# Kernel optimization log

Measured on AMD Instinct MI355X. Metric: run time of the kernel, lower is better.

## Reference

```python
import jax, jax.numpy as jnp
import numpy as np

LEAK = 0.95
NUM_STEPS = 10
THR = 1.0  # all layers get threshold = 1.0 in __init__

@jax.custom_vjp
def spike(x):
    # Surrogate_BP_Function.forward: heaviside(x > 0)
    return (x > 0).astype(x.dtype)

def _spike_fwd(x):
    return spike(x), x

def _spike_bwd(x, g):
    # backward: grad * 0.3 * relu(1 - |x|)
    return (g * 0.3 * jnp.maximum(1.0 - jnp.abs(x), 0.0),)

spike.defvjp(_spike_fwd, _spike_bwd)

def conv3x3(x, w):
    # stride 1, padding 1, no bias, NCHW / OIHW
    return jax.lax.conv_general_dilated(
        x, w, window_strides=(1, 1), padding=[(1, 1), (1, 1)],
        dimension_numbers=('NCHW', 'OIHW', 'NCHW'))

def avgpool2(x):
    b, c, h, w = x.shape
    return x.reshape(b, c, h // 2, 2, w // 2, 2).mean(axis=(3, 5))

def setup_inputs() -> dict:
    key = jax.random.key(0)
    ks = jax.random.split(key, 11)
    def w(k, shape, scale):
        return jax.random.normal(k, shape, dtype=jnp.float32) * scale
    inp = jax.random.normal(ks[0], (128, 3, 32, 32), dtype=jnp.float32)
    return {
        'inp': inp,
        'w1': w(ks[1], (64, 3, 3, 3), 0.35),
        'w2': w(ks[2], (64, 64, 3, 3), 0.1),
        'w3': w(ks[3], (128, 64, 3, 3), 0.1),
        'w4': w(ks[4], (128, 128, 3, 3), 0.08),
        'w5': w(ks[5], (256, 128, 3, 3), 0.08),
        'w6': w(ks[6], (256, 256, 3, 3), 0.06),
        'w7': w(ks[7], (256, 256, 3, 3), 0.06),
        'fc1_w': w(ks[8], (1024, 4096), 0.03),   # Linear(4*4*256, 1024)
        'fc2_w': w(ks[9], (10, 1024), 0.05),     # Linear(1024, 10)
    }

def reference(inp, w1, w2, w3, w4, w5, w6, w7, fc1_w, fc2_w):
    batch = inp.shape[0]
    conv_ws = [w2, w3, w4, w5, w6, w7]          # layers i = 1..6
    pool_after = [True, False, True, False, False, True]  # pool1 after i=1, pool2 after i=3, pool3 after i=6
    static = conv3x3(inp, w1)                   # static_input = conv1(inp)

    def step(carry, _):
        mem0, mem_fc1, mem_fc2 = carry
        # LIF update for conv1 (leaky accumulation of static input)
        mem0 = (1.0 - LEAK) * mem0 + LEAK * static
        thr = mem0 / THR - 1.0
        out_prev = spike(thr)
        mem0 = mem0 - jnp.where(thr > 0, THR, 0.0)  # soft reset
        # conv layers 2..7: membrane is OVERWRITTEN by the conv output each step
        for j, w in enumerate(conv_ws):
            m = conv3x3(out_prev, w)
            thr = m / THR - 1.0
            out_prev = spike(thr)
            if pool_after[j]:
                out_prev = avgpool2(out_prev)
        flat = out_prev.reshape(batch, -1)      # [B, 256*4*4]
        mem_fc1 = (1.0 - LEAK) * mem_fc1 + LEAK * (flat @ fc1_w.T)
        thr = mem_fc1 / THR - 1.0
        out = spike(thr)
        mem_fc1 = mem_fc1 - jnp.where(thr > 0, THR, 0.0)
        mem_fc2 = mem_fc2 + out @ fc2_w.T
        return (mem0, mem_fc1, mem_fc2), None

    init = (jnp.zeros_like(static),
            jnp.zeros((batch, 1024), dtype=inp.dtype),
            jnp.zeros((batch, fc2_w.shape[0]), dtype=inp.dtype))
    (mem0, mem_fc1, mem_fc2), _ = jax.lax.scan(step, init, None, length=NUM_STEPS)
    return mem_fc2 / NUM_STEPS
```

## Files before the change

kernel.cpp:

```cpp
#include <hip/hip_runtime.h>


typedef __attribute__((ext_vector_type(4))) int int32x4;

__device__ __forceinline__ float bf2f(ushort h) {
    union { unsigned u; float f; } v; v.u = ((unsigned)h) << 16;
    return v.f;
}
constexpr int ilog2(int x) { int r = 0; while (x > 1) { x >>= 1; ++r; } return r; }

__device__ __forceinline__ void gl_lds16(const void* g, void* l) {
    __builtin_amdgcn_global_load_lds(
        (const __attribute__((address_space(1))) unsigned int*)g,
        (__attribute__((address_space(3))) unsigned int*)l, 16, 0, 0);
}

#define SC21 4.76837158203125e-07
#define SC23 1.1920928955078125e-07

template <int IC, int OC>
__global__ void prep_convw_i8_k(const float* __restrict__ w, char* __restrict__ dst) {
    int idx = blockIdx.x * 256 + threadIdx.x;
    if (idx >= OC * IC * 9) return;
    int oc = idx / (IC * 9);
    int rem = idx % (IC * 9);
    int ic = rem / 9, q = rem % 9;
    int wq_ = (int)rintf(w[idx] * 2097152.0f);
    int a2 = ((wq_ + 128) & 255) - 128;
    int t2 = (wq_ - a2) >> 8;
    int a1 = ((t2 + 128) & 255) - 128;
    int a0 = (t2 - a1) >> 8;
    int sg = ic >> 6, kin = ic & 63, c = kin >> 4, bb = kin & 15;
    int oct = oc >> 6, ocl = oc & 63;
    constexpr int OCT = OC / 64;
    size_t base = ((size_t)(sg * 9 + q) * OCT + oct) * 12288;
    char digs[3] = {(char)a0, (char)a1, (char)a2};
#pragma unroll
    for (int s = 0; s < 3; ++s)
        dst[base + (size_t)(c * 192 + s * 64 + ocl) * 16 + bb] = digs[s];
}

__global__ void prep_fc1w_i8_k(const float* __restrict__ w, char* __restrict__ dst) {
    int idx = blockIdx.x * 256 + threadIdx.x;
    if (idx >= 1024 * 4096) return;
    int j = idx >> 12, k = idx & 4095;
    int c = k >> 4, hw = k & 15;
    int kp = hw * 256 + c;
    int wq_ = (int)rintf(w[idx] * 2097152.0f);
    int a2 = ((wq_ + 128) & 255) - 128;
    int t2 = (wq_ - a2) >> 8;
    int a1 = ((t2 + 128) & 255) - 128;
    int a0 = (t2 - a1) >> 8;
    int slab = kp >> 6, kin = kp & 63, cch = kin >> 4, bb = kin & 15;
    int oct = j >> 6, ocl = j & 63;
    size_t base = ((size_t)(slab * 16 + oct)) * 12288;
    char digs[3] = {(char)a0, (char)a1, (char)a2};
#pragma unroll
    for (int s = 0; s < 3; ++s)
        dst[base + (size_t)(cch * 192 + s * 64 + ocl) * 16 + bb] = digs[s];
}

template <int H, int C>
__global__ void halo0_k(char* __restrict__ buf) {
    constexpr int P = 4 * H + 4;
    constexpr int CPI = P * (C / 16);
    int idx = blockIdx.x * 256 + threadIdx.x;
    if (idx >= 1280 * CPI) return;
    int n = idx / CPI, r = idx % CPI;
    int p = r / (C / 16), c16 = r % (C / 16);
    int row, col;
    if (p < 2 * (H + 2)) { row = (p < H + 2) ? 0 : H + 1; col = p % (H + 2); }
    else { int qq = p - 2 * (H + 2); col = (qq < H) ? 0 : H + 1; row = 1 + (qq % H); }
    *(uint4*)&buf[(((size_t)n * (H + 2) + row) * (H + 2) + col) * C + c16 * 16] =
        (uint4){0u, 0u, 0u, 0u};
}

__global__ __launch_bounds__(256) void conv1lif_k(const float* __restrict__ inp,
                                                  const float* __restrict__ w1,
                                                  char* __restrict__ act1) {
    __shared__ float ws[27 * 64];
    for (int e = threadIdx.x; e < 1728; e += 256) {
        int oc = e / 27, j = e % 27;
        ws[j * 64 + oc] = w1[e];
    }
    __syncthreads();
    int t = blockIdx.x * 256 + threadIdx.x;
    int q = t & 3;
    int m = t >> 2;
    int n = m >> 10, h = (m >> 5) & 31, w = m & 31;
    float xv[27];
#pragma unroll
    for (int ic = 0; ic < 3; ++ic)
#pragma unroll
        for (int kh = 0; kh < 3; ++kh)
#pragma unroll
            for (int kw = 0; kw < 3; ++kw) {
                int r = h + kh - 1, c = w + kw - 1;
                xv[ic * 9 + kh * 3 + kw] =
                    (r >= 0 && r < 32 && c >= 0 && c < 32)
                        ? inp[(n * 3 + ic) * 1024 + r * 32 + c] : 0.0f;
            }
    float s[16], mem[16];
#pragma unroll
    for (int o = 0; o < 16; ++o) { s[o] = 0.f; mem[o] = 0.f; }
#pragma unroll
    for (int j = 0; j < 27; ++j) {
        float x = xv[j];
        const float* wr = &ws[j * 64 + q * 16];
#pragma unroll
        for (int o = 0; o < 16; ++o) s[o] += wr[o] * x;
    }
    const size_t dbase = (((size_t)h + 1) * 34 + (w + 1)) * 64 + q * 16;
    for (int st = 0; st < 10; ++st) {
        unsigned r[4];
#pragma unroll
        for (int g = 0; g < 4; ++g) {
            unsigned acc = 0;
#pragma unroll
            for (int e = 0; e < 4; ++e) {
                int o = g * 4 + e;
                mem[o] = 0.05f * mem[o] + 0.95f * s[o];
                unsigned b = (mem[o] > 1.f) ? 1u : 0u;
                mem[o] -= (float)b;
                acc |= b << (8 * e);
            }
            r[g] = acc;
        }
        size_t d = ((size_t)(st * 128 + n) * 34 * 34) * 64 + dbase;
        *(uint4*)&act1[d] = (uint4){r[0], r[1], r[2], r[3]};
    }
}

template <int H, int W, int IC, int OC, int NI, int MR, int EPI>
__global__ __launch_bounds__(256) void convi8_k(const char* __restrict__ act,
                                                const char* __restrict__ wq,
                                                char* __restrict__ outs,
                                                float scale) {
    constexpr int PW = W + 2, PHR = MR + 2;
    constexpr int MBLK = NI * MR * W;
    constexpr int NPIX = NI * PHR * PW;
    constexpr int ACH = NPIX * 4;
    constexpr int HR = (ACH + 255) / 256;
    constexpr int SLABS = IC / 64;
    constexpr int OCT = OC / 64;
    constexpr int LHW = ilog2(H * W), LW2 = ilog2(W), LMW = ilog2(MR * W);
    static_assert(MBLK == 128, "tile mapping");

    __shared__ __align__(16) char sA[NPIX * 64];
    __shared__ __align__(16) char sB[2][12288];

    const int tid = threadIdx.x, lane = tid & 63;
    const int wid = tid >> 6, wm = wid >> 1, wn = wid & 1;
    const int b = blockIdx.x, oct = blockIdx.y;
    const int oc0 = oct * 64;
    const int m0 = b * MBLK;
    constexpr int TPI = (NI == 1) ? (H / MR) : 1;
    const int n0 = (NI == 1) ? (b / TPI) : (b * NI);
    const int h0 = (NI == 1) ? (b % TPI) * MR : 0;

    int asrc[HR]; bool apred[HR];
#pragma unroll
    for (int r = 0; r < HR; ++r) {
        int i = r * 256 + tid;
        apred[r] = (i < ACH);
        int ii = apred[r] ? i : 0;
        int c = ii / NPIX, pix = ii % NPIX;
        int pc = pix % PW, t2 = pix / PW;
        int hp = t2 % PHR, img = t2 / PHR;
        asrc[r] = (((n0 + img) * (H + 2) + h0 + hp) * PW + pc) * IC + c * 16;
    }
    int apix[4];
#pragma unroll
    for (int am = 0; am < 4; ++am) {
        int p = wm * 64 + am * 16 + (lane & 15);
        int img = p >> LMW;
        int pi = p & ((MR * W) - 1);
        int h = pi >> LW2;
        apix[am] = (img * PHR + h) * PW + (pi & (W - 1));
    }
    const int cA = lane >> 4;

    int32x4 acc[3][4][2];
#pragma unroll
    for (int s = 0; s < 3; ++s)
#pragma unroll
        for (int a = 0; a < 4; ++a)
#pragma unroll
            for (int bn = 0; bn < 2; ++bn) acc[s][a][bn] = (int32x4){0, 0, 0, 0};

    const size_t wqoct = (size_t)oct * 12288;
    int buf = 0;
    {
#pragma unroll
        for (int r = 0; r < HR; ++r)
            if (apred[r]) gl_lds16(act + asrc[r], sA + (r * 256 + tid) * 16);
        const char* wsrc = wq + wqoct + tid * 16;
#pragma unroll
        for (int r = 0; r < 3; ++r)
            gl_lds16(wsrc + r * 4096, sB[0] + (r * 256 + tid) * 16);
    }
    __syncthreads();

    for (int sl = 0; sl < SLABS; ++sl) {
        for (int q = 0; q < 9; ++q) {
            if (q < 8) {
                const char* wsrc = wq + (size_t)(sl * 9 + q + 1) * OCT * 12288 + wqoct + tid * 16;
#pragma unroll
                for (int r = 0; r < 3; ++r)
                    gl_lds16(wsrc + r * 4096, sB[buf ^ 1] + (r * 256 + tid) * 16);
            }
            const int qr = q / 3, qc = q % 3;
            int32x4 af[4];
#pragma unroll
            for (int am = 0; am < 4; ++am) {
                int pix = apix[am] + qr * PW + qc;
                af[am] = *(const int32x4*)&sA[(cA * NPIX + pix) * 16];
            }
#pragma unroll
            for (int s = 0; s < 3; ++s)
#pragma unroll
                for (int bn = 0; bn < 2; ++bn) {
                    int R = s * 64 + wn * 32 + bn * 16 + (lane & 15);
                    int32x4 bf = *(const int32x4*)&sB[buf][(cA * 192 + R) * 16];
#pragma unroll
                    for (int am = 0; am < 4; ++am)
                        acc[s][am][bn] = __builtin_amdgcn_mfma_i32_16x16x64_i8(
                            af[am], bf, acc[s][am][bn], 0, 0, 0);
                }
            if (q < 8) {
                __syncthreads();
                buf ^= 1;
            }
        }
        if (sl + 1 < SLABS) {
            const int sg2 = sl + 1;
            __syncthreads();
#pragma unroll
            for (int r = 0; r < HR; ++r)
                if (apred[r]) gl_lds16(act + asrc[r] + sg2 * 64, sA + (r * 256 + tid) * 16);
            const char* wsrc = wq + (size_t)(sg2 * 9) * OCT * 12288 + wqoct + tid * 16;
#pragma unroll
            for (int r = 0; r < 3; ++r)
                gl_lds16(wsrc + r * 4096, sB[buf ^ 1] + (r * 256 + tid) * 16);
            __syncthreads();
            buf ^= 1;
        }
    }

    const double dscale = (double)scale;
#pragma unroll
    for (int am = 0; am < 4; ++am)
#pragma unroll
        for (int bn = 0; bn < 2; ++bn)
#pragma unroll
            for (int rr = 0; rr < 4; ++rr) {
                int rl = wm * 64 + am * 16 + (lane >> 4) * 4 + rr;
                int col = oc0 + wn * 32 + bn * 16 + (lane & 15);
                int m = m0 + rl;
                float v = (float)((65536.0 * (double)acc[0][am][bn][rr]
                                 + 256.0 * (double)acc[1][am][bn][rr]
                                 + (double)acc[2][am][bn][rr]) * dscale);
                char sp = (v > 1.0f) ? (char)1 : (char)0;
                if (EPI == 1) {
                    int n = m >> LHW, h = (m >> LW2) & (H - 1), w = m & (W - 1);
                    outs[((size_t)(n * (H + 2) + h + 1) * PW + (w + 1)) * OC + col] = sp;
                } else {
                    outs[(size_t)m * OC + col] = sp;
                }
            }
}

template <int C, int HI>
__global__ void pool_i8_k(const char* __restrict__ in, char* __restrict__ out) {
    constexpr int HO = HI / 2, C16 = C / 16;
    constexpr int TOT = 1280 * HO * HO * C16;
    int idx = blockIdx.x * 256 + threadIdx.x;
    if (idx >= TOT) return;
    int c16 = idx % C16;
    int t = idx / C16;
    int w = t % HO; t /= HO;
    int h = t % HO;
    int n = t / HO;
    const char* p = in + ((size_t)(n * HI + 2 * h) * HI + 2 * w) * C + c16 * 16;
    uint4 a0 = *(const uint4*)p;
    uint4 a1 = *(const uint4*)(p + C);
    uint4 a2 = *(const uint4*)(p + (size_t)HI * C);
    uint4 a3 = *(const uint4*)(p + (size_t)HI * C + C);
    uint4 r;
    r.x = a0.x + a1.x + a2.x + a3.x;
    r.y = a0.y + a1.y + a2.y + a3.y;
    r.z = a0.z + a1.z + a2.z + a3.z;
    r.w = a0.w + a1.w + a2.w + a3.w;
    *(uint4*)&out[((size_t)(n * (HO + 2) + h + 1) * (HO + 2) + (w + 1)) * C + c16 * 16] = r;
}

__global__ void pool3q_k(const char* __restrict__ in, char* __restrict__ out) {
    int idx = blockIdx.x * 256 + threadIdx.x;
    if (idx >= 327680) return;
    int c16 = idx & 15;
    int t = idx >> 4;
    int wo = t & 3, ho = (t >> 2) & 3, n = t >> 4;
    const char* p = in + ((size_t)(n * 8 + 2 * ho) * 8 + 2 * wo) * 256 + c16 * 16;
    uint4 a0 = *(const uint4*)p;
    uint4 a1 = *(const uint4*)(p + 256);
    uint4 a2 = *(const uint4*)(p + 2048);
    uint4 a3 = *(const uint4*)(p + 2048 + 256);
    uint4 r;
    r.x = a0.x + a1.x + a2.x + a3.x;
    r.y = a0.y + a1.y + a2.y + a3.y;
    r.z = a0.z + a1.z + a2.z + a3.z;
    r.w = a0.w + a1.w + a2.w + a3.w;
    *(uint4*)&out[((size_t)(n * 16 + ho * 4 + wo) * 16 + c16) * 16] = r;
}

__global__ __launch_bounds__(256) void fc1i8_k(const char* __restrict__ A,
                                               const char* __restrict__ wq,
                                               float* __restrict__ part) {
    __shared__ __align__(16) char sA[2][8192];
    __shared__ __align__(16) char sB[2][12288];
    const int tid = threadIdx.x, lane = tid & 63;
    const int wid = tid >> 6, wm = wid >> 1, wn = wid & 1;
    const int m0 = blockIdx.x * 128, oct = blockIdx.y, kt = blockIdx.z;

    int32x4 acc[3][4][2];
#pragma unroll
    for (int s = 0; s < 3; ++s)
#pragma unroll
        for (int a = 0; a < 4; ++a)
#pragma unroll
            for (int bn = 0; bn < 2; ++bn) acc[s][a][bn] = (int32x4){0, 0, 0, 0};

    auto stageA = [&](int sg, int bf_) {
#pragma unroll
        for (int r = 0; r < 2; ++r) {
            int i = r * 256 + tid;
            int c = i >> 7, pix = i & 127;
            gl_lds16(A + (size_t)(m0 + pix) * 4096 + sg * 64 + c * 16,
                     sA[bf_] + (size_t)i * 16);
        }
    };
    auto stageB = [&](int sg, int bf_) {
        const char* src = wq + ((size_t)(sg * 16 + oct)) * 12288 + tid * 16;
#pragma unroll
        for (int r = 0; r < 3; ++r)
            gl_lds16(src + r * 4096, sB[bf_] + (r * 256 + tid) * 16);
    };

    int buf = 0;
    stageA(kt * 32, 0);
    stageB(kt * 32, 0);
    __syncthreads();
    const int cA = lane >> 4;
    for (int sl = 0; sl < 32; ++sl) {
        int sg = kt * 32 + sl;
        if (sl < 31) { stageA(sg + 1, buf ^ 1); stageB(sg + 1, buf ^ 1); }
        int32x4 af[4];
#pragma unroll
        for (int am = 0; am < 4; ++am)
            af[am] = *(const int32x4*)&sA[buf][(cA * 128 + wm * 64 + am * 16 + (lane & 15)) * 16];
#pragma unroll
        for (int s = 0; s < 3; ++s)
#pragma unroll
            for (int bn = 0; bn < 2; ++bn) {
                int R = s * 64 + wn * 32 + bn * 16 + (lane & 15);
                int32x4 bf = *(const int32x4*)&sB[buf][(cA * 192 + R) * 16];
#pragma unroll
                for (int am = 0; am < 4; ++am)
                    acc[s][am][bn] = __builtin_amdgcn_mfma_i32_16x16x64_i8(
                        af[am], bf, acc[s][am][bn], 0, 0, 0);
            }
        if (sl < 31) { __syncthreads(); buf ^= 1; }
    }
#pragma unroll
    for (int am = 0; am < 4; ++am)
#pragma unroll
        for (int bn = 0; bn < 2; ++bn)
#pragma unroll
            for (int rr = 0; rr < 4; ++rr) {
                int row = m0 + wm * 64 + am * 16 + (lane >> 4) * 4 + rr;
                int col = oct * 64 + wn * 32 + bn * 16 + (lane & 15);
                float v = (float)((65536.0 * (double)acc[0][am][bn][rr]
                                 + 256.0 * (double)acc[1][am][bn][rr]
                                 + (double)acc[2][am][bn][rr]) * SC23);
                part[((size_t)kt * 1280 + row) * 1024 + col] = v;
            }
}

__global__ void fc1lif_k(const float* __restrict__ part, ushort* __restrict__ sbuf) {
    int idx = blockIdx.x * 256 + threadIdx.x;
    int n = idx >> 10, j = idx & 1023;
    float m = 0.f;
    for (int t = 0; t < 10; ++t) {
        size_t row = (size_t)(t * 128 + n) * 1024 + j;
        float y = part[row] + part[1310720 + row];
        m = 0.05f * m + 0.95f * y;
        float sp = (m > 1.f) ? 1.f : 0.f;
        m -= sp;
        sbuf[row] = sp > 0.f ? (ushort)0x3F80 : (ushort)0;
    }
}

__global__ __launch_bounds__(256) void fc2o_k(const ushort* __restrict__ S,
                                              const float* __restrict__ W2,
                                              float* __restrict__ out) {
    __shared__ float wsh[10 * 1024];
    __shared__ float red[10][256];
    int n = blockIdx.x, tid = threadIdx.x;
    for (int e = tid; e < 10240; e += 256) wsh[e] = W2[e];
    __syncthreads();
    float accv = 0.f;
    for (int t = 0; t < 10; ++t) {
        const ushort* sp = S + ((size_t)(t * 128 + n)) * 1024 + tid * 4;
        float s0 = bf2f(sp[0]), s1 = bf2f(sp[1]), s2 = bf2f(sp[2]), s3 = bf2f(sp[3]);
#pragma unroll
        for (int o = 0; o < 10; ++o) {
            const float* w = &wsh[o * 1024 + tid * 4];
            red[o][tid] = s0 * w[0] + s1 * w[1] + s2 * w[2] + s3 * w[3];
        }
        __syncthreads();
        for (int off = 128; off >= 1; off >>= 1) {
            if (tid < off) {
#pragma unroll
                for (int o = 0; o < 10; ++o) red[o][tid] += red[o][tid + off];
            }
            __syncthreads();
        }
        if (tid < 10) accv += red[tid][0];
        __syncthreads();
    }
    if (tid < 10) out[n * 10 + tid] = accv * 0.1f;
}

extern "C" void kernel_launch(void* const* d_in, const int* in_sizes, int n_in,
                              void* d_out, int out_size, void* d_ws, size_t ws_size,
                              hipStream_t stream) {
    const float* inp  = (const float*)d_in[0];
    const float* w1   = (const float*)d_in[1];
    const float* w2   = (const float*)d_in[2];
    const float* w3   = (const float*)d_in[3];
    const float* w4   = (const float*)d_in[4];
    const float* w5   = (const float*)d_in[5];
    const float* w6   = (const float*)d_in[6];
    const float* w7   = (const float*)d_in[7];
    const float* fc1w = (const float*)d_in[8];
    const float* fc2w = (const float*)d_in[9];
    float* out = (float*)d_out;

    char* base = (char*)d_ws;
    char* arenaA = base;
    char* arenaB = base + 94679040;
    size_t o = 94679040 + 83886080;
    auto alloc = [&](size_t bytes) { void* p = base + o; o += (bytes + 255) & ~(size_t)255; return p; };
    char*   wq2  = (char*)alloc(110592);
    char*   wq3  = (char*)alloc(221184);
    char*   wq4  = (char*)alloc(442368);
    char*   wq5  = (char*)alloc(884736);
    char*   wq6  = (char*)alloc(1769472);
    char*   wq7  = (char*)alloc(1769472);
    char*   wqf1 = (char*)alloc(12582912);
    ushort* sbuf = (ushort*)alloc(2621440);
    (void)ws_size;

    char*  act1  = arenaA;
    char*  c2out = arenaB;
    char*  act2  = arenaA;
    char*  c3out = arenaB;
    char*  c4out = arenaA;
    char*  act3  = arenaA + 41943040;
    char*  c5out = arenaB;
    char*  c6out = arenaB + 33554432;
    char*  c7out = arenaA;
    char*  afc1  = arenaA + 20971520;
    float* part  = (float*)(arenaA + 26214400);

    prep_convw_i8_k<64, 64>  <<<(36864 + 255) / 256, 256, 0, stream>>>(w2, wq2);
    prep_convw_i8_k<64, 128> <<<(73728 + 255) / 256, 256, 0, stream>>>(w3, wq3);
    prep_convw_i8_k<128, 128><<<(147456 + 255) / 256, 256, 0, stream>>>(w4, wq4);
    prep_convw_i8_k<128, 256><<<(294912 + 255) / 256, 256, 0, stream>>>(w5, wq5);
    prep_convw_i8_k<256, 256><<<(589824 + 255) / 256, 256, 0, stream>>>(w6, wq6);
    prep_convw_i8_k<256, 256><<<(589824 + 255) / 256, 256, 0, stream>>>(w7, wq7);
    prep_fc1w_i8_k<<<(4194304 + 255) / 256, 256, 0, stream>>>(fc1w, wqf1);

    halo0_k<32, 64><<<(1280 * 132 * 4 + 255) / 256, 256, 0, stream>>>(act1);
    conv1lif_k<<<2048, 256, 0, stream>>>(inp, w1, act1);

    convi8_k<32, 32, 64, 64, 1, 4, 0>
        <<<dim3(10240, 1), 256, 0, stream>>>(act1, wq2, c2out, (float)SC21);
    halo0_k<16, 64><<<(1280 * 68 * 4 + 255) / 256, 256, 0, stream>>>(act2);
    pool_i8_k<64, 32><<<(1280 * 256 * 4 + 255) / 256, 256, 0, stream>>>(c2out, act2);

    halo0_k<16, 128><<<(1280 * 68 * 8 + 255) / 256, 256, 0, stream>>>(c3out);
    convi8_k<16, 16, 64, 128, 1, 8, 1>
        <<<dim3(2560, 2), 256, 0, stream>>>(act2, wq3, c3out, (float)SC23);
    convi8_k<16, 16, 128, 128, 1, 8, 0>
        <<<dim3(2560, 2), 256, 0, stream>>>(c3out, wq4, c4out, (float)SC21);
    halo0_k<8, 128><<<(1280 * 36 * 8 + 255) / 256, 256, 0, stream>>>(act3);
    pool_i8_k<128, 16><<<(1280 * 64 * 8 + 255) / 256, 256, 0, stream>>>(c4out, act3);

    halo0_k<8, 256><<<(1280 * 36 * 16 + 255) / 256, 256, 0, stream>>>(c5out);
    convi8_k<8, 8, 128, 256, 2, 8, 1>
        <<<dim3(640, 4), 256, 0, stream>>>(act3, wq5, c5out, (float)SC23);
    halo0_k<8, 256><<<(1280 * 36 * 16 + 255) / 256, 256, 0, stream>>>(c6out);
    convi8_k<8, 8, 256, 256, 2, 8, 1>
        <<<dim3(640, 4), 256, 0, stream>>>(c5out, wq6, c6out, (float)SC21);
    convi8_k<8, 8, 256, 256, 2, 8, 0>
        <<<dim3(640, 4), 256, 0, stream>>>(c6out, wq7, c7out, (float)SC21);

    pool3q_k<<<(327680 + 255) / 256, 256, 0, stream>>>(c7out, afc1);

    fc1i8_k<<<dim3(10, 16, 2), 256, 0, stream>>>(afc1, wqf1, part);
    fc1lif_k<<<512, 256, 0, stream>>>(part, sbuf);
    fc2o_k<<<128, 256, 0, stream>>>(sbuf, fc2w, out);
}
```

Baseline: 899.3 us.

## Triple-buffer conv weight tiles with a flattened loop and manual waitcnt barriers

The int8 conv kernel's weight staging moves from double to triple buffering, with prefetch two steps ahead. The slab/tap double loop becomes a single flattened loop. __syncthreads is replaced by explicit vmcnt waits plus s_barrier, so each iteration needs only one barrier instead of two. MFMA issue is wrapped in s_setprio. The extra 12KB of LDS per block may reduce occupancy, and the hand-written waitcnt counts must match the number of outstanding loads exactly.

```diff
diff --git a/kernel.cpp b/kernel.cpp
--- a/kernel.cpp
+++ b/kernel.cpp
@@ -143,11 +143,12 @@
     constexpr int HR = (ACH + 255) / 256;
     constexpr int SLABS = IC / 64;
     constexpr int OCT = OC / 64;
+    constexpr int U = SLABS * 9;
     constexpr int LHW = ilog2(H * W), LW2 = ilog2(W), LMW = ilog2(MR * W);
     static_assert(MBLK == 128, "tile mapping");
 
     __shared__ __align__(16) char sA[NPIX * 64];
-    __shared__ __align__(16) char sB[2][12288];
+    __shared__ __align__(16) char sB[3][12288];
 
     const int tid = threadIdx.x, lane = tid & 63;
     const int wid = tid >> 6, wm = wid >> 1, wn = wid & 1;
@@ -189,65 +190,62 @@
             for (int bn = 0; bn < 2; ++bn) acc[s][a][bn] = (int32x4){0, 0, 0, 0};
 
     const size_t wqoct = (size_t)oct * 12288;
-    int buf = 0;
-    {
+
+    auto stage_B = [&](int u_) {
+        const char* wsrc = wq + (size_t)u_ * (OCT * 12288) + wqoct + tid * 16;
+        char* d = sB[u_ % 3] + tid * 16;
+        gl_lds16(wsrc, d);
+        gl_lds16(wsrc + 4096, d + 4096);
+        gl_lds16(wsrc + 8192, d + 8192);
+    };
+    auto stage_A = [&](int sl_) {
 #pragma unroll
         for (int r = 0; r < HR; ++r)
-            if (apred[r]) gl_lds16(act + asrc[r], sA + (r * 256 + tid) * 16);
-        const char* wsrc = wq + wqoct + tid * 16;
-#pragma unroll
-        for (int r = 0; r < 3; ++r)
-            gl_lds16(wsrc + r * 4096, sB[0] + (r * 256 + tid) * 16);
-    }
-    __syncthreads();
-
-    for (int sl = 0; sl < SLABS; ++sl) {
-        for (int q = 0; q < 9; ++q) {
-            if (q < 8) {
-                const char* wsrc = wq + (size_t)(sl * 9 + q + 1) * OCT * 12288 + wqoct + tid * 16;
-#pragma unroll
-                for (int r = 0; r < 3; ++r)
-                    gl_lds16(wsrc + r * 4096, sB[buf ^ 1] + (r * 256 + tid) * 16);
-            }
-            const int qr = q / 3, qc = q % 3;
-            int32x4 af[4];
-#pragma unroll
-            for (int am = 0; am < 4; ++am) {
-                int pix = apix[am] + qr * PW + qc;
-                af[am] = *(const int32x4*)&sA[(cA * NPIX + pix) * 16];
-            }
-#pragma unroll
-            for (int s = 0; s < 3; ++s)
-#pragma unroll
-                for (int bn = 0; bn < 2; ++bn) {
-                    int R = s * 64 + wn * 32 + bn * 16 + (lane & 15);
-                    int32x4 bf = *(const int32x4*)&sB[buf][(cA * 192 + R) * 16];
-#pragma unroll
-                    for (int am = 0; am < 4; ++am)
-                        acc[s][am][bn] = __builtin_amdgcn_mfma_i32_16x16x64_i8(
-                            af[am], bf, acc[s][am][bn], 0, 0, 0);
-                }
-            if (q < 8) {
-                __syncthreads();
-                buf ^= 1;
-            }
+            if (apred[r]) gl_lds16(act + asrc[r] + sl_ * 64, sA + (r * 256 + tid) * 16);
+    };
+
+    stage_A(0);
+    stage_B(0);
+    stage_B(1);
+
+    for (int u = 0; u < U; ++u) {
+        const int q = u - (u / 9) * 9;
+        if (q == 0) asm volatile("s_waitcnt vmcnt(0)" ::: "memory");
+        else        asm volatile("s_waitcnt vmcnt(3)" ::: "memory");
+        __builtin_amdgcn_s_barrier();
+        asm volatile("" ::: "memory");
+        if (u + 2 < U) stage_B(u + 2);
+
+        const int qr = q / 3, qc = q - qr * 3;
+        int32x4 af[4];
+#pragma unroll
+        for (int am = 0; am < 4; ++am) {
+            int pix = apix[am] + qr * PW + qc;
+            af[am] = *(const int32x4*)&sA[(cA * NPIX + pix) * 16];
         }
-        if (sl + 1 < SLABS) {
-            const int sg2 = sl + 1;
-            __syncthreads();
-#pragma unroll
-            for (int r = 0; r < HR; ++r)
-                if (apred[r]) gl_lds16(act + asrc[r] + sg2 * 64, sA + (r * 256 + tid) * 16);
-            const char* wsrc = wq + (size_t)(sg2 * 9) * OCT * 12288 + wqoct + tid * 16;
-#pragma unroll
-            for (int r = 0; r < 3; ++r)
-                gl_lds16(wsrc + r * 4096, sB[buf ^ 1] + (r * 256 + tid) * 16);
-            __syncthreads();
-            buf ^= 1;
+        const char* bbase = sB[u % 3];
+        __builtin_amdgcn_s_setprio(1);
+#pragma unroll
+        for (int s = 0; s < 3; ++s)
+#pragma unroll
+            for (int bn = 0; bn < 2; ++bn) {
+                int R = s * 64 + wn * 32 + bn * 16 + (lane & 15);
+                int32x4 bf = *(const int32x4*)&bbase[(cA * 192 + R) * 16];
+#pragma unroll
+                for (int am = 0; am < 4; ++am)
+                    acc[s][am][bn] = __builtin_amdgcn_mfma_i32_16x16x64_i8(
+                        af[am], bf, acc[s][am][bn], 0, 0, 0);
+            }
+        __builtin_amdgcn_s_setprio(0);
+
+        if (q == 8 && u + 1 < U) {
+            asm volatile("s_waitcnt lgkmcnt(0)" ::: "memory");
+            __builtin_amdgcn_s_barrier();
+            asm volatile("" ::: "memory");
+            stage_A(u / 9 + 1);
         }
     }
 
-    const double dscale = (double)scale;
 #pragma unroll
     for (int am = 0; am < 4; ++am)
 #pragma unroll
@@ -259,7 +257,7 @@
                 int m = m0 + rl;
                 float v = (float)((65536.0 * (double)acc[0][am][bn][rr]
                                  + 256.0 * (double)acc[1][am][bn][rr]
-                                 + (double)acc[2][am][bn][rr]) * dscale);
+                                 + (double)acc[2][am][bn][rr]) * (double)scale);
                 char sp = (v > 1.0f) ? (char)1 : (char)0;
                 if (EPI == 1) {
                     int n = m >> LHW, h = (m >> LW2) & (H - 1), w = m & (W - 1);
```

Measured after the change: 887.4 us. Within noise of the previous version (-1.3%).
